# Kernel tuning notes

Measured on AMD Instinct MI355X. Metric: run time of the kernel, lower is better.

Reference implementation:

```python
import jax, jax.numpy as jnp
import numpy as np

B, NIN, NOUT, K = 1024, 126, 126, 3
H1, H2 = 256, 256

def _linear_params(key, out_f, in_f):
    # torch nn.Linear default init: U(-1/sqrt(in_f), 1/sqrt(in_f))
    bound = 1.0 / np.sqrt(in_f)
    kw, kb = jax.random.split(key)
    W = jax.random.uniform(kw, (out_f, in_f), minval=-bound, maxval=bound, dtype=jnp.float32)
    b = jax.random.uniform(kb, (out_f,), minval=-bound, maxval=bound, dtype=jnp.float32)
    return W, b

def setup_inputs() -> dict:
    key = jax.random.key(0)
    k0, k1, k2, kx, ki, ko = jax.random.split(key, 6)
    W0, b0 = _linear_params(k0, H1, NIN)
    W1, b1 = _linear_params(k1, H2, H1)
    W2, b2 = _linear_params(k2, NOUT, H2)
    x = jax.random.normal(kx, (B, NIN), dtype=jnp.float32)
    batch_in_index = jax.random.randint(ki, (B, NIN, K), 0, NIN + 1)   # NIN is zero-pad row
    batch_out_index = jax.random.randint(ko, (B, NOUT, K), 0, NOUT + 1)  # NOUT is zero-pad row
    return dict(x=x, W0=W0, b0=b0, W1=W1, b1=b1, W2=W2, b2=b2,
                batch_in_index=batch_in_index, batch_out_index=batch_out_index)

def reference(x, W0, b0, W1, b1, W2, b2, batch_in_index, batch_out_index):
    # --- layer 0: BatchIndexedLinear with batch_in_index ---
    # padded weight: (nin+1, h1), last row zeros
    pw0 = jnp.concatenate([W0.T, jnp.zeros((1, W0.shape[0]), W0.dtype)], axis=0)
    bw0 = pw0[batch_in_index].sum(-2)                 # (B, nin, h1)
    h = jnp.einsum('bi,bio->bo', x, bw0) + b0          # (B, h1)
    h = jax.nn.elu(h)
    # --- layer 1: plain linear ---
    h = jax.nn.elu(h @ W1.T + b1)                      # (B, h2)
    # --- layer 2: BatchIndexedLinear with batch_out_index ---
    pw2 = jnp.concatenate([W2, jnp.zeros((1, W2.shape[1]), W2.dtype)], axis=0)  # (nout+1, h2)
    g = pw2[batch_out_index].sum(-2)                   # (B, nout, h2)
    pb2 = jnp.concatenate([b2, jnp.zeros((1,), b2.dtype)])
    bb = pb2[batch_out_index].sum(-1)                  # (B, nout)
    return jnp.einsum('bh,boh->bo', h, g) + bb         # (B, nout)
```

## Files before the change

### kernel.cpp

```cpp
#include <hip/hip_runtime.h>

#define B_    1024
#define NIN_  126
#define NOUT_ 126
#define K_    3
#define H1_   256
#define H2_   256
#define RPB   4
#define TPB   512

__device__ __forceinline__ float elu1(float v) { return v > 0.0f ? v : expm1f(v); }

template<int CTRL>
__device__ __forceinline__ float dpp_add(float v) {
    int s = __builtin_amdgcn_update_dpp(0, __float_as_int(v), CTRL, 0xF, 0xF, true);
    return v + __int_as_float(s);
}
__device__ __forceinline__ float qsum8(float v) {
    v = dpp_add<0xB1>(v);
    v = dpp_add<0x4E>(v);
    int s = __builtin_amdgcn_ds_swizzle(__float_as_int(v), 0x101F);
    return v + __int_as_float(s);
}

__device__ __forceinline__ void barrier_lds() {
    asm volatile("s_waitcnt lgkmcnt(0)\n\ts_barrier" ::: "memory");
}

__global__ __launch_bounds__(TPB, 2) void bim_fused(
    const float* __restrict__ x,  const float* __restrict__ W0,
    const float* __restrict__ b0, const float* __restrict__ W1,
    const float* __restrict__ b1, const float* __restrict__ W2,
    const float* __restrict__ b2, const int*  __restrict__ iidx,
    const int*  __restrict__ oidx, float* __restrict__ out)
{
    __shared__ float xe [RPB][128];
    __shared__ float h1s[RPB][H1_];
    __shared__ float h2s[RPB][H2_];
    __shared__ float ts [RPB][128];

    const int tid  = threadIdx.x;
    const int row0 = blockIdx.x * RPB;
    const int q    = tid & 7;
    const int g    = tid >> 3;

    int aj0, aj1, aj2, ar0, ar1, ar2; float ax0, ax1, ax2;
    {
        const int n0 = tid;
        ar0 = n0 / (NIN_ * K_); const int m0 = n0 - ar0 * (NIN_ * K_);
        aj0 = iidx[(row0 + ar0) * (NIN_ * K_) + m0];
        ax0 = x[(row0 + ar0) * NIN_ + m0 / K_];
        const int n1 = tid + TPB;
        ar1 = n1 / (NIN_ * K_); const int m1 = n1 - ar1 * (NIN_ * K_);
        aj1 = iidx[(row0 + ar1) * (NIN_ * K_) + m1];
        ax1 = x[(row0 + ar1) * NIN_ + m1 / K_];
        const int n2 = tid + 2 * TPB;
        const int n2c = n2 < RPB * NIN_ * K_ ? n2 : 0;
        ar2 = n2c / (NIN_ * K_); const int m2 = n2c - ar2 * (NIN_ * K_);
        aj2 = iidx[(row0 + ar2) * (NIN_ * K_) + m2];
        ax2 = x[(row0 + ar2) * NIN_ + m2 / K_];
        if (n2 >= RPB * NIN_ * K_) aj2 = NIN_;
    }
    int ej0, ej1, ej2;
    {
        const int t = tid < RPB * NOUT_ ? tid : 0;
        const int r = t / NOUT_, o = t - r * NOUT_;
        const int base = (row0 + r) * (NOUT_ * K_) + o * K_;
        ej0 = oidx[base]; ej1 = oidx[base + 1]; ej2 = oidx[base + 2];
    }
    float2 wbA[4][4], wbB[4][4];
    #pragma unroll
    for (int oo = 0; oo < 4; ++oo) {
        const float* wp = W0 + (g * 4 + oo) * NIN_;
        #pragma unroll
        for (int jj = 0; jj < 4; ++jj) {
            const int j  = q * 4 + jj * 32;
            const int j2 = (j + 2 > NIN_ - 2) ? (NIN_ - 2) : (j + 2);
            wbA[jj][oo] = *reinterpret_cast<const float2*>(wp + j);
            wbB[jj][oo] = *reinterpret_cast<const float2*>(wp + j2);
        }
    }
    const float4 b0v = *reinterpret_cast<const float4*>(b0 + g * 4);
    const float4 b1v = *reinterpret_cast<const float4*>(b1 + g * 4);
    const int   gD   = (g < 63) ? g : 0;
    const float2 b2v = *reinterpret_cast<const float2*>(b2 + gD * 2);

    (&xe[0][0])[tid] = 0.0f;
    barrier_lds();
    if (aj0 < NIN_) atomicAdd(&xe[ar0][aj0], ax0);
    if (aj1 < NIN_) atomicAdd(&xe[ar1][aj1], ax1);
    if (aj2 < NIN_) atomicAdd(&xe[ar2][aj2], ax2);

    float4 wc[8][4];
    #pragma unroll
    for (int oo = 0; oo < 4; ++oo) {
        const float* wp = W1 + (g * 4 + oo) * H1_;
        #pragma unroll
        for (int jj = 0; jj < 8; ++jj)
            wc[jj][oo] = *reinterpret_cast<const float4*>(wp + q * 4 + jj * 32);
    }
    barrier_lds();

    {
        float acc[4][4] = {};
        #pragma unroll
        for (int jj = 0; jj < 4; ++jj) {
            const int j = q * 4 + jj * 32;
            #pragma unroll
            for (int r = 0; r < RPB; ++r) {
                const float4 a = *reinterpret_cast<const float4*>(&xe[r][j]);
                #pragma unroll
                for (int oo = 0; oo < 4; ++oo) {
                    acc[oo][r] = fmaf(wbA[jj][oo].x, a.x, acc[oo][r]);
                    acc[oo][r] = fmaf(wbA[jj][oo].y, a.y, acc[oo][r]);
                    acc[oo][r] = fmaf(wbB[jj][oo].x, a.z, acc[oo][r]);
                    acc[oo][r] = fmaf(wbB[jj][oo].y, a.w, acc[oo][r]);
                }
            }
        }
        #pragma unroll
        for (int oo = 0; oo < 4; ++oo)
            #pragma unroll
            for (int r = 0; r < RPB; ++r) acc[oo][r] = qsum8(acc[oo][r]);
        float v0 = acc[0][0], v1 = acc[0][1];
        #pragma unroll
        for (int i = 1; i < 8; ++i) {
            v0 = (q == i) ? acc[(2 * i) >> 2][(2 * i) & 3]         : v0;
            v1 = (q == i) ? acc[(2 * i + 1) >> 2][(2 * i + 1) & 3] : v1;
        }
        const int oo = q >> 1, r0 = (q & 1) * 2;
        const float bias = (oo == 0) ? b0v.x : (oo == 1) ? b0v.y : (oo == 2) ? b0v.z : b0v.w;
        const int o = g * 4 + oo;
        h1s[r0][o]     = elu1(v0 + bias);
        h1s[r0 + 1][o] = elu1(v1 + bias);
    }
    barrier_lds();

    float4 wd[8][2];
    {
        float acc[4][4] = {};
        #pragma unroll
        for (int jj = 0; jj < 8; ++jj) {
            const int j = q * 4 + jj * 32;
            #pragma unroll
            for (int r = 0; r < RPB; ++r) {
                const float4 a = *reinterpret_cast<const float4*>(&h1s[r][j]);
                #pragma unroll
                for (int oo = 0; oo < 4; ++oo) {
                    acc[oo][r] = fmaf(wc[jj][oo].x, a.x, acc[oo][r]);
                    acc[oo][r] = fmaf(wc[jj][oo].y, a.y, acc[oo][r]);
                    acc[oo][r] = fmaf(wc[jj][oo].z, a.z, acc[oo][r]);
                    acc[oo][r] = fmaf(wc[jj][oo].w, a.w, acc[oo][r]);
                }
            }
        }
        #pragma unroll
        for (int oo = 0; oo < 2; ++oo) {
            const float* wp = W2 + (gD * 2 + oo) * H2_;
            #pragma unroll
            for (int jj = 0; jj < 8; ++jj)
                wd[jj][oo] = *reinterpret_cast<const float4*>(wp + q * 4 + jj * 32);
        }
        #pragma unroll
        for (int oo = 0; oo < 4; ++oo)
            #pragma unroll
            for (int r = 0; r < RPB; ++r) acc[oo][r] = qsum8(acc[oo][r]);
        float v0 = acc[0][0], v1 = acc[0][1];
        #pragma unroll
        for (int i = 1; i < 8; ++i) {
            v0 = (q == i) ? acc[(2 * i) >> 2][(2 * i) & 3]         : v0;
            v1 = (q == i) ? acc[(2 * i + 1) >> 2][(2 * i + 1) & 3] : v1;
        }
        const int oo = q >> 1, r0 = (q & 1) * 2;
        const float bias = (oo == 0) ? b1v.x : (oo == 1) ? b1v.y : (oo == 2) ? b1v.z : b1v.w;
        const int o = g * 4 + oo;
        h2s[r0][o]     = elu1(v0 + bias);
        h2s[r0 + 1][o] = elu1(v1 + bias);
    }
    barrier_lds();

    {
        float acc[2][4] = {};
        #pragma unroll
        for (int jj = 0; jj < 8; ++jj) {
            const int j = q * 4 + jj * 32;
            #pragma unroll
            for (int r = 0; r < RPB; ++r) {
                const float4 a = *reinterpret_cast<const float4*>(&h2s[r][j]);
                #pragma unroll
                for (int oo = 0; oo < 2; ++oo) {
                    acc[oo][r] = fmaf(wd[jj][oo].x, a.x, acc[oo][r]);
                    acc[oo][r] = fmaf(wd[jj][oo].y, a.y, acc[oo][r]);
                    acc[oo][r] = fmaf(wd[jj][oo].z, a.z, acc[oo][r]);
                    acc[oo][r] = fmaf(wd[jj][oo].w, a.w, acc[oo][r]);
                }
            }
        }
        #pragma unroll
        for (int oo = 0; oo < 2; ++oo)
            #pragma unroll
            for (int r = 0; r < RPB; ++r) acc[oo][r] = qsum8(acc[oo][r]);
        float v = acc[0][0];
        #pragma unroll
        for (int i = 1; i < 8; ++i) v = (q == i) ? acc[i >> 2][i & 3] : v;
        const int oo = q >> 2, rr = q & 3;
        if (g < 63) ts[rr][g * 2 + oo] = v + (oo ? b2v.y : b2v.x);
        else        ts[rr][126 + oo]   = 0.0f;
    }
    barrier_lds();

    if (tid < RPB * NOUT_) {
        const int r = tid / NOUT_, o = tid - r * NOUT_;
        out[(row0 + r) * NOUT_ + o] = ts[r][ej0] + ts[r][ej1] + ts[r][ej2];
    }
}

extern "C" void kernel_launch(void* const* d_in, const int* in_sizes, int n_in,
                              void* d_out, int out_size, void* d_ws, size_t ws_size,
                              hipStream_t stream) {
    const float* x   = (const float*)d_in[0];
    const float* W0  = (const float*)d_in[1];
    const float* b0  = (const float*)d_in[2];
    const float* W1  = (const float*)d_in[3];
    const float* b1  = (const float*)d_in[4];
    const float* W2  = (const float*)d_in[5];
    const float* b2  = (const float*)d_in[6];
    const int*  iidx = (const int*)d_in[7];
    const int*  oidx = (const int*)d_in[8];
    float* out = (float*)d_out;

    bim_fused<<<B_ / RPB, TPB, 0, stream>>>(x, W0, b0, W1, b1, W2, b2, iidx, oidx, out);
}
```

Baseline: 16.33 us.

## Stream weight tiles with one-step register prefetch instead of bulk preloading

The kernel used to load each layer's whole weight slice into registers up front. It now loads one 32-column chunk at a time and prefetches the next chunk while the current one is used in FMAs. It also drops the min-blocks hint from launch_bounds. This cuts register pressure, which could raise occupancy and avoid spills, but it gives up the early overlap of W1 and W2 loads with the previous layer's work and the atomic scatter, so more global load latency may be exposed inside each loop.

```diff
diff --git a/kernel.cpp b/kernel.cpp
--- a/kernel.cpp
+++ b/kernel.cpp
@@ -27,7 +27,7 @@
     asm volatile("s_waitcnt lgkmcnt(0)\n\ts_barrier" ::: "memory");
 }
 
-__global__ __launch_bounds__(TPB, 2) void bim_fused(
+__global__ __launch_bounds__(TPB) void bim_fused(
     const float* __restrict__ x,  const float* __restrict__ W0,
     const float* __restrict__ b0, const float* __restrict__ W1,
     const float* __restrict__ b1, const float* __restrict__ W2,
@@ -68,56 +68,69 @@
         const int base = (row0 + r) * (NOUT_ * K_) + o * K_;
         ej0 = oidx[base]; ej1 = oidx[base + 1]; ej2 = oidx[base + 2];
     }
-    float2 wbA[4][4], wbB[4][4];
-    #pragma unroll
-    for (int oo = 0; oo < 4; ++oo) {
-        const float* wp = W0 + (g * 4 + oo) * NIN_;
-        #pragma unroll
-        for (int jj = 0; jj < 4; ++jj) {
-            const int j  = q * 4 + jj * 32;
-            const int j2 = (j + 2 > NIN_ - 2) ? (NIN_ - 2) : (j + 2);
-            wbA[jj][oo] = *reinterpret_cast<const float2*>(wp + j);
-            wbB[jj][oo] = *reinterpret_cast<const float2*>(wp + j2);
-        }
-    }
     const float4 b0v = *reinterpret_cast<const float4*>(b0 + g * 4);
     const float4 b1v = *reinterpret_cast<const float4*>(b1 + g * 4);
-    const int   gD   = (g < 63) ? g : 0;
+    const int    gD  = (g < 63) ? g : 0;
     const float2 b2v = *reinterpret_cast<const float2*>(b2 + gD * 2);
+
+    const float* wb = W0 + (g * 4) * NIN_;
+    float2 wA[4], wB[4];
+    {
+        const int j = q * 4;
+        const int j2 = (j + 2 > NIN_ - 2) ? (NIN_ - 2) : (j + 2);
+        #pragma unroll
+        for (int oo = 0; oo < 4; ++oo) {
+            wA[oo] = *reinterpret_cast<const float2*>(wb + oo * NIN_ + j);
+            wB[oo] = *reinterpret_cast<const float2*>(wb + oo * NIN_ + j2);
+        }
+    }
 
     (&xe[0][0])[tid] = 0.0f;
     barrier_lds();
     if (aj0 < NIN_) atomicAdd(&xe[ar0][aj0], ax0);
     if (aj1 < NIN_) atomicAdd(&xe[ar1][aj1], ax1);
     if (aj2 < NIN_) atomicAdd(&xe[ar2][aj2], ax2);
-
-    float4 wc[8][4];
-    #pragma unroll
-    for (int oo = 0; oo < 4; ++oo) {
-        const float* wp = W1 + (g * 4 + oo) * H1_;
-        #pragma unroll
-        for (int jj = 0; jj < 8; ++jj)
-            wc[jj][oo] = *reinterpret_cast<const float4*>(wp + q * 4 + jj * 32);
-    }
-    barrier_lds();
-
+    barrier_lds();
+
+    const float* wcp = W1 + (g * 4) * H1_ + q * 4;
+    float4 wc[4];
     {
         float acc[4][4] = {};
         #pragma unroll
         for (int jj = 0; jj < 4; ++jj) {
+            float2 nA[4], nB[4];
+            if (jj < 3) {
+                const int j = q * 4 + (jj + 1) * 32;
+                const int j2 = (j + 2 > NIN_ - 2) ? (NIN_ - 2) : (j + 2);
+                #pragma unroll
+                for (int oo = 0; oo < 4; ++oo) {
+                    nA[oo] = *reinterpret_cast<const float2*>(wb + oo * NIN_ + j);
+                    nB[oo] = *reinterpret_cast<const float2*>(wb + oo * NIN_ + j2);
+                }
+            }
             const int j = q * 4 + jj * 32;
-            #pragma unroll
-            for (int r = 0; r < RPB; ++r) {
-                const float4 a = *reinterpret_cast<const float4*>(&xe[r][j]);
-                #pragma unroll
-                for (int oo = 0; oo < 4; ++oo) {
-                    acc[oo][r] = fmaf(wbA[jj][oo].x, a.x, acc[oo][r]);
-                    acc[oo][r] = fmaf(wbA[jj][oo].y, a.y, acc[oo][r]);
-                    acc[oo][r] = fmaf(wbB[jj][oo].x, a.z, acc[oo][r]);
-                    acc[oo][r] = fmaf(wbB[jj][oo].y, a.w, acc[oo][r]);
-                }
-            }
-        }
+            float4 a[RPB];
+            #pragma unroll
+            for (int r = 0; r < RPB; ++r)
+                a[r] = *reinterpret_cast<const float4*>(&xe[r][j]);
+            #pragma unroll
+            for (int oo = 0; oo < 4; ++oo)
+                #pragma unroll
+                for (int r = 0; r < RPB; ++r) {
+                    acc[oo][r] = fmaf(wA[oo].x, a[r].x, acc[oo][r]);
+                    acc[oo][r] = fmaf(wA[oo].y, a[r].y, acc[oo][r]);
+                    acc[oo][r] = fmaf(wB[oo].x, a[r].z, acc[oo][r]);
+                    acc[oo][r] = fmaf(wB[oo].y, a[r].w, acc[oo][r]);
+                }
+            if (jj < 3) {
+                #pragma unroll
+                for (int oo = 0; oo < 4; ++oo) { wA[oo] = nA[oo]; wB[oo] = nB[oo]; }
+            }
+        }
+        #pragma unroll
+        for (int oo = 0; oo < 4; ++oo)
+            wc[oo] = *reinterpret_cast<const float4*>(wcp + oo * H1_);
+
         #pragma unroll
         for (int oo = 0; oo < 4; ++oo)
             #pragma unroll
@@ -136,31 +149,40 @@
     }
     barrier_lds();
 
-    float4 wd[8][2];
+    const float* wdp = W2 + (gD * 2) * H2_ + q * 4;
+    float4 wd[2];
     {
         float acc[4][4] = {};
         #pragma unroll
         for (int jj = 0; jj < 8; ++jj) {
+            float4 nc[4];
+            if (jj < 7) {
+                #pragma unroll
+                for (int oo = 0; oo < 4; ++oo)
+                    nc[oo] = *reinterpret_cast<const float4*>(wcp + oo * H1_ + (jj + 1) * 32);
+            }
             const int j = q * 4 + jj * 32;
-            #pragma unroll
-            for (int r = 0; r < RPB; ++r) {
-                const float4 a = *reinterpret_cast<const float4*>(&h1s[r][j]);
-                #pragma unroll
-                for (int oo = 0; oo < 4; ++oo) {
-                    acc[oo][r] = fmaf(wc[jj][oo].x, a.x, acc[oo][r]);
-                    acc[oo][r] = fmaf(wc[jj][oo].y, a.y, acc[oo][r]);
-                    acc[oo][r] = fmaf(wc[jj][oo].z, a.z, acc[oo][r]);
-                    acc[oo][r] = fmaf(wc[jj][oo].w, a.w, acc[oo][r]);
-                }
-            }
-        }
-        #pragma unroll
-        for (int oo = 0; oo < 2; ++oo) {
-            const float* wp = W2 + (gD * 2 + oo) * H2_;
-            #pragma unroll
-            for (int jj = 0; jj < 8; ++jj)
-                wd[jj][oo] = *reinterpret_cast<const float4*>(wp + q * 4 + jj * 32);
-        }
+            float4 a[RPB];
+            #pragma unroll
+            for (int r = 0; r < RPB; ++r)
+                a[r] = *reinterpret_cast<const float4*>(&h1s[r][j]);
+            #pragma unroll
+            for (int oo = 0; oo < 4; ++oo)
+                #pragma unroll
+                for (int r = 0; r < RPB; ++r) {
+                    acc[oo][r] = fmaf(wc[oo].x, a[r].x, acc[oo][r]);
+                    acc[oo][r] = fmaf(wc[oo].y, a[r].y, acc[oo][r]);
+                    acc[oo][r] = fmaf(wc[oo].z, a[r].z, acc[oo][r]);
+                    acc[oo][r] = fmaf(wc[oo].w, a[r].w, acc[oo][r]);
+                }
+            if (jj < 7) {
+                #pragma unroll
+                for (int oo = 0; oo < 4; ++oo) wc[oo] = nc[oo];
+            }
+        }
+        wd[0] = *reinterpret_cast<const float4*>(wdp);
+        wd[1] = *reinterpret_cast<const float4*>(wdp + H2_);
+
         #pragma unroll
         for (int oo = 0; oo < 4; ++oo)
             #pragma unroll
@@ -183,18 +205,26 @@
         float acc[2][4] = {};
         #pragma unroll
         for (int jj = 0; jj < 8; ++jj) {
+            float4 nd[2];
+            if (jj < 7) {
+                nd[0] = *reinterpret_cast<const float4*>(wdp + (jj + 1) * 32);
+                nd[1] = *reinterpret_cast<const float4*>(wdp + H2_ + (jj + 1) * 32);
+            }
             const int j = q * 4 + jj * 32;
-            #pragma unroll
-            for (int r = 0; r < RPB; ++r) {
-                const float4 a = *reinterpret_cast<const float4*>(&h2s[r][j]);
-                #pragma unroll
-                for (int oo = 0; oo < 2; ++oo) {
-                    acc[oo][r] = fmaf(wd[jj][oo].x, a.x, acc[oo][r]);
-                    acc[oo][r] = fmaf(wd[jj][oo].y, a.y, acc[oo][r]);
-                    acc[oo][r] = fmaf(wd[jj][oo].z, a.z, acc[oo][r]);
-                    acc[oo][r] = fmaf(wd[jj][oo].w, a.w, acc[oo][r]);
-                }
-            }
+            float4 a[RPB];
+            #pragma unroll
+            for (int r = 0; r < RPB; ++r)
+                a[r] = *reinterpret_cast<const float4*>(&h2s[r][j]);
+            #pragma unroll
+            for (int oo = 0; oo < 2; ++oo)
+                #pragma unroll
+                for (int r = 0; r < RPB; ++r) {
+                    acc[oo][r] = fmaf(wd[oo].x, a[r].x, acc[oo][r]);
+                    acc[oo][r] = fmaf(wd[oo].y, a[r].y, acc[oo][r]);
+                    acc[oo][r] = fmaf(wd[oo].z, a[r].z, acc[oo][r]);
+                    acc[oo][r] = fmaf(wd[oo].w, a[r].w, acc[oo][r]);
+                }
+            if (jj < 7) { wd[0] = nd[0]; wd[1] = nd[1]; }
         }
         #pragma unroll
         for (int oo = 0; oo < 2; ++oo)
```

After: 15.83 us. 1.03x faster.

## Convert weights to bf16 in a prepass, halve rows per block, and software-pipeline weight loads

Applied to the files above, without the earlier changes.

Adds a conversion kernel that writes W0, W1 and W2 as bf16 into the workspace. The fused kernel then reads half as many weight bytes, processes 2 rows per block instead of 4 (doubling the grid), raises occupancy via launch bounds, and streams W1/W2 chunks in an interleaved issue/compute order instead of holding them all in registers. This trades a second kernel launch and reduced weight precision for lower register pressure and less weight traffic per block. bf16 rounding of the weights may loosen accuracy against the fp32 reference.

```diff
diff --git a/kernel.cpp b/kernel.cpp
--- a/kernel.cpp
+++ b/kernel.cpp
@@ -6,8 +6,13 @@
 #define K_    3
 #define H1_   256
 #define H2_   256
-#define RPB   4
+#define RPB   2
 #define TPB   512
+
+#define W0BF_OFF 0
+#define W1BF_OFF 32768
+#define W2BF_OFF 98304
+#define WBF_TOTAL 130560
 
 __device__ __forceinline__ float elu1(float v) { return v > 0.0f ? v : expm1f(v); }
 
@@ -22,17 +27,46 @@
     int s = __builtin_amdgcn_ds_swizzle(__float_as_int(v), 0x101F);
     return v + __int_as_float(s);
 }
-
+__device__ __forceinline__ float sel8(int q, float a0, float a1, float a2, float a3,
+                                      float a4, float a5, float a6, float a7) {
+    float v = a0;
+    v = (q == 1) ? a1 : v;  v = (q == 2) ? a2 : v;  v = (q == 3) ? a3 : v;
+    v = (q == 4) ? a4 : v;  v = (q == 5) ? a5 : v;  v = (q == 6) ? a6 : v;
+    v = (q == 7) ? a7 : v;
+    return v;
+}
 __device__ __forceinline__ void barrier_lds() {
     asm volatile("s_waitcnt lgkmcnt(0)\n\ts_barrier" ::: "memory");
 }
-
-__global__ __launch_bounds__(TPB, 2) void bim_fused(
-    const float* __restrict__ x,  const float* __restrict__ W0,
-    const float* __restrict__ b0, const float* __restrict__ W1,
-    const float* __restrict__ b1, const float* __restrict__ W2,
-    const float* __restrict__ b2, const int*  __restrict__ iidx,
-    const int*  __restrict__ oidx, float* __restrict__ out)
+__device__ __forceinline__ unsigned short f2bf(float f) {
+    unsigned u = __float_as_uint(f);
+    u = (u + 0x7FFFu + ((u >> 16) & 1u)) >> 16;
+    return (unsigned short)u;
+}
+__device__ __forceinline__ float2 bf2f(unsigned u) {
+    return make_float2(__uint_as_float(u << 16), __uint_as_float(u & 0xFFFF0000u));
+}
+
+__global__ __launch_bounds__(256) void wconv(
+    const float* __restrict__ W0, const float* __restrict__ W1,
+    const float* __restrict__ W2, unsigned short* __restrict__ wsb)
+{
+    const int t = blockIdx.x * 256 + threadIdx.x;
+    if (t < 32768) {
+        const int o = t >> 7, j = t & 127;
+        wsb[W0BF_OFF + t] = (j < NIN_) ? f2bf(W0[o * NIN_ + j]) : (unsigned short)0;
+    } else if (t < 98304) {
+        wsb[W1BF_OFF + (t - 32768)] = f2bf(W1[t - 32768]);
+    } else if (t < WBF_TOTAL) {
+        wsb[W2BF_OFF + (t - 98304)] = f2bf(W2[t - 98304]);
+    }
+}
+
+__global__ __launch_bounds__(TPB, 4) void bim_fused(
+    const float* __restrict__ x,  const unsigned short* __restrict__ wsb,
+    const float* __restrict__ b0, const float* __restrict__ b1,
+    const float* __restrict__ b2, const int* __restrict__ iidx,
+    const int* __restrict__ oidx, float* __restrict__ out)
 {
     __shared__ float xe [RPB][128];
     __shared__ float h1s[RPB][H1_];
@@ -44,23 +78,40 @@
     const int q    = tid & 7;
     const int g    = tid >> 3;
 
-    int aj0, aj1, aj2, ar0, ar1, ar2; float ax0, ax1, ax2;
+    int aj0, ar0, aj1, ar1; float ax0, ax1;
     {
         const int n0 = tid;
         ar0 = n0 / (NIN_ * K_); const int m0 = n0 - ar0 * (NIN_ * K_);
         aj0 = iidx[(row0 + ar0) * (NIN_ * K_) + m0];
         ax0 = x[(row0 + ar0) * NIN_ + m0 / K_];
         const int n1 = tid + TPB;
-        ar1 = n1 / (NIN_ * K_); const int m1 = n1 - ar1 * (NIN_ * K_);
+        const bool v1 = n1 < RPB * NIN_ * K_;
+        const int n1c = v1 ? n1 : 0;
+        ar1 = n1c / (NIN_ * K_); const int m1 = n1c - ar1 * (NIN_ * K_);
         aj1 = iidx[(row0 + ar1) * (NIN_ * K_) + m1];
         ax1 = x[(row0 + ar1) * NIN_ + m1 / K_];
-        const int n2 = tid + 2 * TPB;
-        const int n2c = n2 < RPB * NIN_ * K_ ? n2 : 0;
-        ar2 = n2c / (NIN_ * K_); const int m2 = n2c - ar2 * (NIN_ * K_);
-        aj2 = iidx[(row0 + ar2) * (NIN_ * K_) + m2];
-        ax2 = x[(row0 + ar2) * NIN_ + m2 / K_];
-        if (n2 >= RPB * NIN_ * K_) aj2 = NIN_;
-    }
+        if (!v1) aj1 = NIN_;
+    }
+
+    const unsigned short* w0b = wsb + W0BF_OFF + (g * 4) * 128 + q * 4;
+    uint2 wb[4][4];
+    #pragma unroll
+    for (int jj = 0; jj < 4; ++jj)
+        #pragma unroll
+        for (int oo = 0; oo < 4; ++oo)
+            wb[jj][oo] = *reinterpret_cast<const uint2*>(w0b + oo * 128 + jj * 32);
+
+    const unsigned short* wcp = wsb + W1BF_OFF + (g * 4) * H1_ + q * 4;
+    uint2 c0[4], c1[4];
+    #pragma unroll
+    for (int oo = 0; oo < 4; ++oo) c0[oo] = *reinterpret_cast<const uint2*>(wcp + oo * H1_);
+    #pragma unroll
+    for (int oo = 0; oo < 4; ++oo) c1[oo] = *reinterpret_cast<const uint2*>(wcp + oo * H1_ + 32);
+
+    const float4 b0v = *reinterpret_cast<const float4*>(b0 + g * 4);
+    const float4 b1v = *reinterpret_cast<const float4*>(b1 + g * 4);
+    const int    gD  = (g < 63) ? g : 0;
+    const float2 b2v = *reinterpret_cast<const float2*>(b2 + gD * 2);
     int ej0, ej1, ej2;
     {
         const int t = tid < RPB * NOUT_ ? tid : 0;
@@ -68,144 +119,133 @@
         const int base = (row0 + r) * (NOUT_ * K_) + o * K_;
         ej0 = oidx[base]; ej1 = oidx[base + 1]; ej2 = oidx[base + 2];
     }
-    float2 wbA[4][4], wbB[4][4];
-    #pragma unroll
-    for (int oo = 0; oo < 4; ++oo) {
-        const float* wp = W0 + (g * 4 + oo) * NIN_;
-        #pragma unroll
-        for (int jj = 0; jj < 4; ++jj) {
-            const int j  = q * 4 + jj * 32;
-            const int j2 = (j + 2 > NIN_ - 2) ? (NIN_ - 2) : (j + 2);
-            wbA[jj][oo] = *reinterpret_cast<const float2*>(wp + j);
-            wbB[jj][oo] = *reinterpret_cast<const float2*>(wp + j2);
-        }
-    }
-    const float4 b0v = *reinterpret_cast<const float4*>(b0 + g * 4);
-    const float4 b1v = *reinterpret_cast<const float4*>(b1 + g * 4);
-    const int   gD   = (g < 63) ? g : 0;
-    const float2 b2v = *reinterpret_cast<const float2*>(b2 + gD * 2);
-
-    (&xe[0][0])[tid] = 0.0f;
+
+    if (tid < RPB * 128) (&xe[0][0])[tid] = 0.0f;
     barrier_lds();
     if (aj0 < NIN_) atomicAdd(&xe[ar0][aj0], ax0);
     if (aj1 < NIN_) atomicAdd(&xe[ar1][aj1], ax1);
-    if (aj2 < NIN_) atomicAdd(&xe[ar2][aj2], ax2);
-
-    float4 wc[8][4];
-    #pragma unroll
-    for (int oo = 0; oo < 4; ++oo) {
-        const float* wp = W1 + (g * 4 + oo) * H1_;
-        #pragma unroll
-        for (int jj = 0; jj < 8; ++jj)
-            wc[jj][oo] = *reinterpret_cast<const float4*>(wp + q * 4 + jj * 32);
-    }
-    barrier_lds();
-
-    {
-        float acc[4][4] = {};
-        #pragma unroll
-        for (int jj = 0; jj < 4; ++jj) {
-            const int j = q * 4 + jj * 32;
-            #pragma unroll
-            for (int r = 0; r < RPB; ++r) {
-                const float4 a = *reinterpret_cast<const float4*>(&xe[r][j]);
-                #pragma unroll
-                for (int oo = 0; oo < 4; ++oo) {
-                    acc[oo][r] = fmaf(wbA[jj][oo].x, a.x, acc[oo][r]);
-                    acc[oo][r] = fmaf(wbA[jj][oo].y, a.y, acc[oo][r]);
-                    acc[oo][r] = fmaf(wbB[jj][oo].x, a.z, acc[oo][r]);
-                    acc[oo][r] = fmaf(wbB[jj][oo].y, a.w, acc[oo][r]);
-                }
-            }
-        }
+    barrier_lds();
+
+#define BSTEP(JJ) { \
+        const float4 a0 = *reinterpret_cast<const float4*>(&xe[0][q * 4 + (JJ) * 32]); \
+        const float4 a1 = *reinterpret_cast<const float4*>(&xe[1][q * 4 + (JJ) * 32]); \
+        _Pragma("unroll") \
+        for (int oo = 0; oo < 4; ++oo) { \
+            const float2 p0 = bf2f(wb[JJ][oo].x); \
+            const float2 p1 = bf2f(wb[JJ][oo].y); \
+            acc[oo][0] = fmaf(p0.x, a0.x, acc[oo][0]); acc[oo][0] = fmaf(p0.y, a0.y, acc[oo][0]); \
+            acc[oo][0] = fmaf(p1.x, a0.z, acc[oo][0]); acc[oo][0] = fmaf(p1.y, a0.w, acc[oo][0]); \
+            acc[oo][1] = fmaf(p0.x, a1.x, acc[oo][1]); acc[oo][1] = fmaf(p0.y, a1.y, acc[oo][1]); \
+            acc[oo][1] = fmaf(p1.x, a1.z, acc[oo][1]); acc[oo][1] = fmaf(p1.y, a1.w, acc[oo][1]); \
+        } }
+#define CSTEP(W, JJ) { \
+        const float4 a0 = *reinterpret_cast<const float4*>(&h1s[0][q * 4 + (JJ) * 32]); \
+        const float4 a1 = *reinterpret_cast<const float4*>(&h1s[1][q * 4 + (JJ) * 32]); \
+        _Pragma("unroll") \
+        for (int oo = 0; oo < 4; ++oo) { \
+            const float2 p0 = bf2f(W[oo].x); \
+            const float2 p1 = bf2f(W[oo].y); \
+            acc[oo][0] = fmaf(p0.x, a0.x, acc[oo][0]); acc[oo][0] = fmaf(p0.y, a0.y, acc[oo][0]); \
+            acc[oo][0] = fmaf(p1.x, a0.z, acc[oo][0]); acc[oo][0] = fmaf(p1.y, a0.w, acc[oo][0]); \
+            acc[oo][1] = fmaf(p0.x, a1.x, acc[oo][1]); acc[oo][1] = fmaf(p0.y, a1.y, acc[oo][1]); \
+            acc[oo][1] = fmaf(p1.x, a1.z, acc[oo][1]); acc[oo][1] = fmaf(p1.y, a1.w, acc[oo][1]); \
+        } }
+#define DSTEP(W, JJ) { \
+        const float4 a0 = *reinterpret_cast<const float4*>(&h2s[0][q * 4 + (JJ) * 32]); \
+        const float4 a1 = *reinterpret_cast<const float4*>(&h2s[1][q * 4 + (JJ) * 32]); \
+        _Pragma("unroll") \
+        for (int oo = 0; oo < 2; ++oo) { \
+            const float2 p0 = bf2f(W[oo].x); \
+            const float2 p1 = bf2f(W[oo].y); \
+            accd[oo][0] = fmaf(p0.x, a0.x, accd[oo][0]); accd[oo][0] = fmaf(p0.y, a0.y, accd[oo][0]); \
+            accd[oo][0] = fmaf(p1.x, a0.z, accd[oo][0]); accd[oo][0] = fmaf(p1.y, a0.w, accd[oo][0]); \
+            accd[oo][1] = fmaf(p0.x, a1.x, accd[oo][1]); accd[oo][1] = fmaf(p0.y, a1.y, accd[oo][1]); \
+            accd[oo][1] = fmaf(p1.x, a1.z, accd[oo][1]); accd[oo][1] = fmaf(p1.y, a1.w, accd[oo][1]); \
+        } }
+#define ISSUE_C(DST, JJ) { _Pragma("unroll") \
+        for (int oo = 0; oo < 4; ++oo) DST[oo] = *reinterpret_cast<const uint2*>(wcp + oo * H1_ + (JJ) * 32); }
+#define ISSUE_D(DST, JJ) { _Pragma("unroll") \
+        for (int oo = 0; oo < 2; ++oo) DST[oo] = *reinterpret_cast<const uint2*>(wdp + oo * H2_ + (JJ) * 32); }
+
+    uint2 c2[4], c3[4];
+    {
+        float acc[4][2] = {};
+        BSTEP(0)
+        ISSUE_C(c2, 2)
+        BSTEP(1)
+        ISSUE_C(c3, 3)
+        BSTEP(2)
+        BSTEP(3)
         #pragma unroll
         for (int oo = 0; oo < 4; ++oo)
             #pragma unroll
             for (int r = 0; r < RPB; ++r) acc[oo][r] = qsum8(acc[oo][r]);
-        float v0 = acc[0][0], v1 = acc[0][1];
-        #pragma unroll
-        for (int i = 1; i < 8; ++i) {
-            v0 = (q == i) ? acc[(2 * i) >> 2][(2 * i) & 3]         : v0;
-            v1 = (q == i) ? acc[(2 * i + 1) >> 2][(2 * i + 1) & 3] : v1;
-        }
-        const int oo = q >> 1, r0 = (q & 1) * 2;
+        const float v = sel8(q, acc[0][0], acc[0][1], acc[1][0], acc[1][1],
+                                acc[2][0], acc[2][1], acc[3][0], acc[3][1]);
+        const int oo = q >> 1, r = q & 1;
         const float bias = (oo == 0) ? b0v.x : (oo == 1) ? b0v.y : (oo == 2) ? b0v.z : b0v.w;
-        const int o = g * 4 + oo;
-        h1s[r0][o]     = elu1(v0 + bias);
-        h1s[r0 + 1][o] = elu1(v1 + bias);
-    }
-    barrier_lds();
-
-    float4 wd[8][2];
-    {
-        float acc[4][4] = {};
-        #pragma unroll
-        for (int jj = 0; jj < 8; ++jj) {
-            const int j = q * 4 + jj * 32;
-            #pragma unroll
-            for (int r = 0; r < RPB; ++r) {
-                const float4 a = *reinterpret_cast<const float4*>(&h1s[r][j]);
-                #pragma unroll
-                for (int oo = 0; oo < 4; ++oo) {
-                    acc[oo][r] = fmaf(wc[jj][oo].x, a.x, acc[oo][r]);
-                    acc[oo][r] = fmaf(wc[jj][oo].y, a.y, acc[oo][r]);
-                    acc[oo][r] = fmaf(wc[jj][oo].z, a.z, acc[oo][r]);
-                    acc[oo][r] = fmaf(wc[jj][oo].w, a.w, acc[oo][r]);
-                }
-            }
-        }
-        #pragma unroll
-        for (int oo = 0; oo < 2; ++oo) {
-            const float* wp = W2 + (gD * 2 + oo) * H2_;
-            #pragma unroll
-            for (int jj = 0; jj < 8; ++jj)
-                wd[jj][oo] = *reinterpret_cast<const float4*>(wp + q * 4 + jj * 32);
-        }
+        h1s[r][g * 4 + oo] = elu1(v + bias);
+    }
+    barrier_lds();
+
+    const unsigned short* wdp = wsb + W2BF_OFF + (gD * 2) * H2_ + q * 4;
+    uint2 c4[4], c5[4], c6[4], c7[4], d0[2], d1[2];
+    {
+        float acc[4][2] = {};
+        CSTEP(c0, 0)
+        ISSUE_C(c4, 4)
+        CSTEP(c1, 1)
+        ISSUE_C(c5, 5)
+        CSTEP(c2, 2)
+        ISSUE_C(c6, 6)
+        CSTEP(c3, 3)
+        ISSUE_C(c7, 7)
+        CSTEP(c4, 4)
+        ISSUE_D(d0, 0)
+        CSTEP(c5, 5)
+        ISSUE_D(d1, 1)
+        CSTEP(c6, 6)
+        CSTEP(c7, 7)
         #pragma unroll
         for (int oo = 0; oo < 4; ++oo)
             #pragma unroll
             for (int r = 0; r < RPB; ++r) acc[oo][r] = qsum8(acc[oo][r]);
-        float v0 = acc[0][0], v1 = acc[0][1];
-        #pragma unroll
-        for (int i = 1; i < 8; ++i) {
-            v0 = (q == i) ? acc[(2 * i) >> 2][(2 * i) & 3]         : v0;
-            v1 = (q == i) ? acc[(2 * i + 1) >> 2][(2 * i + 1) & 3] : v1;
-        }
-        const int oo = q >> 1, r0 = (q & 1) * 2;
+        const float v = sel8(q, acc[0][0], acc[0][1], acc[1][0], acc[1][1],
+                                acc[2][0], acc[2][1], acc[3][0], acc[3][1]);
+        const int oo = q >> 1, r = q & 1;
         const float bias = (oo == 0) ? b1v.x : (oo == 1) ? b1v.y : (oo == 2) ? b1v.z : b1v.w;
-        const int o = g * 4 + oo;
-        h2s[r0][o]     = elu1(v0 + bias);
-        h2s[r0 + 1][o] = elu1(v1 + bias);
-    }
-    barrier_lds();
-
-    {
-        float acc[2][4] = {};
-        #pragma unroll
-        for (int jj = 0; jj < 8; ++jj) {
-            const int j = q * 4 + jj * 32;
-            #pragma unroll
-            for (int r = 0; r < RPB; ++r) {
-                const float4 a = *reinterpret_cast<const float4*>(&h2s[r][j]);
-                #pragma unroll
-                for (int oo = 0; oo < 2; ++oo) {
-                    acc[oo][r] = fmaf(wd[jj][oo].x, a.x, acc[oo][r]);
-                    acc[oo][r] = fmaf(wd[jj][oo].y, a.y, acc[oo][r]);
-                    acc[oo][r] = fmaf(wd[jj][oo].z, a.z, acc[oo][r]);
-                    acc[oo][r] = fmaf(wd[jj][oo].w, a.w, acc[oo][r]);
-                }
-            }
-        }
+        h2s[r][g * 4 + oo] = elu1(v + bias);
+    }
+    barrier_lds();
+
+    {
+        uint2 d2[2], d3[2], d4[2], d5[2], d6[2], d7[2];
+        float accd[2][2] = {};
+        DSTEP(d0, 0)
+        ISSUE_D(d2, 2)
+        DSTEP(d1, 1)
+        ISSUE_D(d3, 3)
+        DSTEP(d2, 2)
+        ISSUE_D(d4, 4)
+        DSTEP(d3, 3)
+        ISSUE_D(d5, 5)
+        DSTEP(d4, 4)
+        ISSUE_D(d6, 6)
+        DSTEP(d5, 5)
+        ISSUE_D(d7, 7)
+        DSTEP(d6, 6)
+        DSTEP(d7, 7)
         #pragma unroll
         for (int oo = 0; oo < 2; ++oo)
             #pragma unroll
-            for (int r = 0; r < RPB; ++r) acc[oo][r] = qsum8(acc[oo][r]);
-        float v = acc[0][0];
-        #pragma unroll
-        for (int i = 1; i < 8; ++i) v = (q == i) ? acc[i >> 2][i & 3] : v;
-        const int oo = q >> 2, rr = q & 3;
-        if (g < 63) ts[rr][g * 2 + oo] = v + (oo ? b2v.y : b2v.x);
-        else        ts[rr][126 + oo]   = 0.0f;
+            for (int r = 0; r < RPB; ++r) accd[oo][r] = qsum8(accd[oo][r]);
+        const float v = sel8(q, accd[0][0], accd[0][1], accd[1][0], accd[1][1],
+                                accd[0][0], accd[0][1], accd[1][0], accd[1][1]);
+        if (q < 4) {
+            const int oo = q >> 1, rr = q & 1;
+            if (g < 63) ts[rr][g * 2 + oo] = v + (oo ? b2v.y : b2v.x);
+            else        ts[rr][126 + oo]   = 0.0f;
+        }
     }
     barrier_lds();
 
@@ -213,6 +253,11 @@
         const int r = tid / NOUT_, o = tid - r * NOUT_;
         out[(row0 + r) * NOUT_ + o] = ts[r][ej0] + ts[r][ej1] + ts[r][ej2];
     }
+#undef BSTEP
+#undef CSTEP
+#undef DSTEP
+#undef ISSUE_C
+#undef ISSUE_D
 }
 
 extern "C" void kernel_launch(void* const* d_in, const int* in_sizes, int n_in,
@@ -228,6 +273,8 @@
     const int*  iidx = (const int*)d_in[7];
     const int*  oidx = (const int*)d_in[8];
     float* out = (float*)d_out;
-
-    bim_fused<<<B_ / RPB, TPB, 0, stream>>>(x, W0, b0, W1, b1, W2, b2, iidx, oidx, out);
-}
+    unsigned short* wsb = (unsigned short*)d_ws;
+
+    wconv<<<512, 256, 0, stream>>>(W0, W1, W2, wsb);
+    bim_fused<<<B_ / RPB, TPB, 0, stream>>>(x, wsb, b0, b1, b2, iidx, oidx, out);
+}
```

Result: slower. 21.39 us (+31.0%).

## Stage W1 through LDS as bf16 with chunked loads overlapped with layer 0

Applied to the files above, without the earlier changes.

Layer 1 weights are no longer held per thread in registers. They are streamed cooperatively from global memory in four coalesced chunks, converted to bf16 and written to a large dynamic LDS buffer. The chunk loads are interleaved with the atomic scatter and the layer-0 FMA steps to hide their latency. Layer 1 then reads packed bf16 weights from LDS. The goal is to cut register pressure and overlap weight traffic with compute, at the cost of bf16 rounding on W1, extra pack/unpack ALU work, and about 150KB of LDS per block, which limits occupancy to one block per CU.

```diff
diff --git a/kernel.cpp b/kernel.cpp
--- a/kernel.cpp
+++ b/kernel.cpp
@@ -8,8 +8,10 @@
 #define H2_   256
 #define RPB   4
 #define TPB   512
-
-__device__ __forceinline__ float elu1(float v) { return v > 0.0f ? v : expm1f(v); }
+#define W1S   276
+#define SMEM_BYTES (256 * W1S * 2 + (RPB * 128 + RPB * H1_ + RPB * H2_ + RPB * 128) * 4)
+
+__device__ __forceinline__ float elu1(float v) { return v > 0.f ? v : expm1f(v); }
 
 template<int CTRL>
 __device__ __forceinline__ float dpp_add(float v) {
@@ -22,27 +24,40 @@
     int s = __builtin_amdgcn_ds_swizzle(__float_as_int(v), 0x101F);
     return v + __int_as_float(s);
 }
-
 __device__ __forceinline__ void barrier_lds() {
     asm volatile("s_waitcnt lgkmcnt(0)\n\ts_barrier" ::: "memory");
 }
-
-__global__ __launch_bounds__(TPB, 2) void bim_fused(
+__device__ __forceinline__ unsigned f2bf(float f) {
+    unsigned u = __float_as_uint(f);
+    return (u + 0x7FFFu + ((u >> 16) & 1u)) >> 16;
+}
+__device__ __forceinline__ unsigned packbf(float a, float b) {
+    return f2bf(a) | (f2bf(b) << 16);
+}
+__device__ __forceinline__ float2 bf2f(unsigned u) {
+    return make_float2(__uint_as_float(u << 16), __uint_as_float(u & 0xFFFF0000u));
+}
+
+__global__ __launch_bounds__(TPB) void bim_fused(
     const float* __restrict__ x,  const float* __restrict__ W0,
     const float* __restrict__ b0, const float* __restrict__ W1,
     const float* __restrict__ b1, const float* __restrict__ W2,
     const float* __restrict__ b2, const int*  __restrict__ iidx,
     const int*  __restrict__ oidx, float* __restrict__ out)
 {
-    __shared__ float xe [RPB][128];
-    __shared__ float h1s[RPB][H1_];
-    __shared__ float h2s[RPB][H2_];
-    __shared__ float ts [RPB][128];
+    extern __shared__ char smem[];
+    unsigned short* w1l = (unsigned short*)smem;
+    float* xe  = (float*)(smem + 256 * W1S * 2);
+    float* h1s = xe  + RPB * 128;
+    float* h2s = h1s + RPB * H1_;
+    float* tsb = h2s + RPB * H2_;
 
     const int tid  = threadIdx.x;
     const int row0 = blockIdx.x * RPB;
     const int q    = tid & 7;
     const int g    = tid >> 3;
+
+    const float4* w1f4 = reinterpret_cast<const float4*>(W1);
 
     int aj0, aj1, aj2, ar0, ar1, ar2; float ax0, ax1, ax2;
     {
@@ -61,6 +76,32 @@
         ax2 = x[(row0 + ar2) * NIN_ + m2 / K_];
         if (n2 >= RPB * NIN_ * K_) aj2 = NIN_;
     }
+
+    const float* wb = W0 + (g * 4) * NIN_;
+    float2 wA[4][4], wB[4][4];
+    #pragma unroll
+    for (int jj = 0; jj < 4; ++jj) {
+        const int j  = q * 4 + jj * 32;
+        const int j2 = (j + 2 > NIN_ - 2) ? (NIN_ - 2) : (j + 2);
+        #pragma unroll
+        for (int oo = 0; oo < 4; ++oo) {
+            wA[jj][oo] = *reinterpret_cast<const float2*>(wb + oo * NIN_ + j);
+            wB[jj][oo] = *reinterpret_cast<const float2*>(wb + oo * NIN_ + j2);
+        }
+    }
+
+    float4 s0[8], s1[8], s2[8], s3[8];
+#define ISSUE_CHUNK(S, P) { _Pragma("unroll") \
+    for (int u = 0; u < 8; ++u) S[u] = w1f4[((P) * 8 + u) * TPB + tid]; }
+#define WRITE_CHUNK(S, P) { _Pragma("unroll") \
+    for (int u = 0; u < 8; ++u) { \
+        const int i4 = ((P) * 8 + u) * TPB + tid; \
+        const int row = i4 >> 6, c4 = i4 & 63; \
+        uint2 pk; pk.x = packbf(S[u].x, S[u].y); pk.y = packbf(S[u].z, S[u].w); \
+        *reinterpret_cast<uint2*>(&w1l[row * W1S + c4 * 4]) = pk; } }
+
+    ISSUE_CHUNK(s0, 0)
+
     int ej0, ej1, ej2;
     {
         const int t = tid < RPB * NOUT_ ? tid : 0;
@@ -68,56 +109,75 @@
         const int base = (row0 + r) * (NOUT_ * K_) + o * K_;
         ej0 = oidx[base]; ej1 = oidx[base + 1]; ej2 = oidx[base + 2];
     }
-    float2 wbA[4][4], wbB[4][4];
-    #pragma unroll
-    for (int oo = 0; oo < 4; ++oo) {
-        const float* wp = W0 + (g * 4 + oo) * NIN_;
-        #pragma unroll
-        for (int jj = 0; jj < 4; ++jj) {
-            const int j  = q * 4 + jj * 32;
-            const int j2 = (j + 2 > NIN_ - 2) ? (NIN_ - 2) : (j + 2);
-            wbA[jj][oo] = *reinterpret_cast<const float2*>(wp + j);
-            wbB[jj][oo] = *reinterpret_cast<const float2*>(wp + j2);
-        }
-    }
     const float4 b0v = *reinterpret_cast<const float4*>(b0 + g * 4);
     const float4 b1v = *reinterpret_cast<const float4*>(b1 + g * 4);
-    const int   gD   = (g < 63) ? g : 0;
+    const int    gD  = (g < 63) ? g : 0;
     const float2 b2v = *reinterpret_cast<const float2*>(b2 + gD * 2);
 
-    (&xe[0][0])[tid] = 0.0f;
-    barrier_lds();
-    if (aj0 < NIN_) atomicAdd(&xe[ar0][aj0], ax0);
-    if (aj1 < NIN_) atomicAdd(&xe[ar1][aj1], ax1);
-    if (aj2 < NIN_) atomicAdd(&xe[ar2][aj2], ax2);
-
-    float4 wc[8][4];
-    #pragma unroll
-    for (int oo = 0; oo < 4; ++oo) {
-        const float* wp = W1 + (g * 4 + oo) * H1_;
-        #pragma unroll
-        for (int jj = 0; jj < 8; ++jj)
-            wc[jj][oo] = *reinterpret_cast<const float4*>(wp + q * 4 + jj * 32);
-    }
-    barrier_lds();
+    xe[tid] = 0.0f;
+    barrier_lds();
+    if (aj0 < NIN_) atomicAdd(&xe[ar0 * 128 + aj0], ax0);
+    if (aj1 < NIN_) atomicAdd(&xe[ar1 * 128 + aj1], ax1);
+    if (aj2 < NIN_) atomicAdd(&xe[ar2 * 128 + aj2], ax2);
+    WRITE_CHUNK(s0, 0)
+    ISSUE_CHUNK(s1, 1)
+    barrier_lds();
+
+#define BSTEP(JJ) { \
+        const int j = q * 4 + (JJ) * 32; \
+        _Pragma("unroll") \
+        for (int r = 0; r < RPB; ++r) { \
+            const float4 a = *reinterpret_cast<const float4*>(&xe[r * 128 + j]); \
+            _Pragma("unroll") \
+            for (int oo = 0; oo < 4; ++oo) { \
+                acc[oo][r] = fmaf(wA[JJ][oo].x, a.x, acc[oo][r]); \
+                acc[oo][r] = fmaf(wA[JJ][oo].y, a.y, acc[oo][r]); \
+                acc[oo][r] = fmaf(wB[JJ][oo].x, a.z, acc[oo][r]); \
+                acc[oo][r] = fmaf(wB[JJ][oo].y, a.w, acc[oo][r]); \
+            } } }
+#define CSTEP(JJ) { \
+        const int j = q * 4 + (JJ) * 32; \
+        float4 a[RPB]; \
+        _Pragma("unroll") \
+        for (int r = 0; r < RPB; ++r) \
+            a[r] = *reinterpret_cast<const float4*>(&h1s[r * H1_ + j]); \
+        _Pragma("unroll") \
+        for (int oo = 0; oo < 4; ++oo) { \
+            const uint2 wv = *reinterpret_cast<const uint2*>(&w1l[(g * 4 + oo) * W1S + j]); \
+            const float2 p0 = bf2f(wv.x), p1 = bf2f(wv.y); \
+            _Pragma("unroll") \
+            for (int r = 0; r < RPB; ++r) { \
+                acc[oo][r] = fmaf(p0.x, a[r].x, acc[oo][r]); \
+                acc[oo][r] = fmaf(p0.y, a[r].y, acc[oo][r]); \
+                acc[oo][r] = fmaf(p1.x, a[r].z, acc[oo][r]); \
+                acc[oo][r] = fmaf(p1.y, a[r].w, acc[oo][r]); \
+            } } }
+#define DSTEP(JJ) { \
+        const int j = q * 4 + (JJ) * 32; \
+        float4 a[RPB]; \
+        _Pragma("unroll") \
+        for (int r = 0; r < RPB; ++r) \
+            a[r] = *reinterpret_cast<const float4*>(&h2s[r * H2_ + j]); \
+        _Pragma("unroll") \
+        for (int oo = 0; oo < 2; ++oo) { \
+            _Pragma("unroll") \
+            for (int r = 0; r < RPB; ++r) { \
+                accd[oo][r] = fmaf(wd[JJ][oo].x, a[r].x, accd[oo][r]); \
+                accd[oo][r] = fmaf(wd[JJ][oo].y, a[r].y, accd[oo][r]); \
+                accd[oo][r] = fmaf(wd[JJ][oo].z, a[r].z, accd[oo][r]); \
+                accd[oo][r] = fmaf(wd[JJ][oo].w, a[r].w, accd[oo][r]); \
+            } } }
 
     {
         float acc[4][4] = {};
-        #pragma unroll
-        for (int jj = 0; jj < 4; ++jj) {
-            const int j = q * 4 + jj * 32;
-            #pragma unroll
-            for (int r = 0; r < RPB; ++r) {
-                const float4 a = *reinterpret_cast<const float4*>(&xe[r][j]);
-                #pragma unroll
-                for (int oo = 0; oo < 4; ++oo) {
-                    acc[oo][r] = fmaf(wbA[jj][oo].x, a.x, acc[oo][r]);
-                    acc[oo][r] = fmaf(wbA[jj][oo].y, a.y, acc[oo][r]);
-                    acc[oo][r] = fmaf(wbB[jj][oo].x, a.z, acc[oo][r]);
-                    acc[oo][r] = fmaf(wbB[jj][oo].y, a.w, acc[oo][r]);
-                }
-            }
-        }
+        BSTEP(0)
+        BSTEP(1)
+        WRITE_CHUNK(s1, 1)
+        ISSUE_CHUNK(s2, 2)
+        BSTEP(2)
+        BSTEP(3)
+        WRITE_CHUNK(s2, 2)
+        ISSUE_CHUNK(s3, 3)
         #pragma unroll
         for (int oo = 0; oo < 4; ++oo)
             #pragma unroll
@@ -131,36 +191,23 @@
         const int oo = q >> 1, r0 = (q & 1) * 2;
         const float bias = (oo == 0) ? b0v.x : (oo == 1) ? b0v.y : (oo == 2) ? b0v.z : b0v.w;
         const int o = g * 4 + oo;
-        h1s[r0][o]     = elu1(v0 + bias);
-        h1s[r0 + 1][o] = elu1(v1 + bias);
-    }
-    barrier_lds();
-
+        h1s[r0 * H1_ + o]       = elu1(v0 + bias);
+        h1s[(r0 + 1) * H1_ + o] = elu1(v1 + bias);
+        WRITE_CHUNK(s3, 3)
+    }
+    const float* wdp = W2 + (gD * 2) * H2_ + q * 4;
     float4 wd[8][2];
+    #pragma unroll
+    for (int jj = 0; jj < 8; ++jj)
+        #pragma unroll
+        for (int oo = 0; oo < 2; ++oo)
+            wd[jj][oo] = *reinterpret_cast<const float4*>(wdp + oo * H2_ + jj * 32);
+    barrier_lds();
+
     {
         float acc[4][4] = {};
-        #pragma unroll
-        for (int jj = 0; jj < 8; ++jj) {
-            const int j = q * 4 + jj * 32;
-            #pragma unroll
-            for (int r = 0; r < RPB; ++r) {
-                const float4 a = *reinterpret_cast<const float4*>(&h1s[r][j]);
-                #pragma unroll
-                for (int oo = 0; oo < 4; ++oo) {
-                    acc[oo][r] = fmaf(wc[jj][oo].x, a.x, acc[oo][r]);
-                    acc[oo][r] = fmaf(wc[jj][oo].y, a.y, acc[oo][r]);
-                    acc[oo][r] = fmaf(wc[jj][oo].z, a.z, acc[oo][r]);
-                    acc[oo][r] = fmaf(wc[jj][oo].w, a.w, acc[oo][r]);
-                }
-            }
-        }
-        #pragma unroll
-        for (int oo = 0; oo < 2; ++oo) {
-            const float* wp = W2 + (gD * 2 + oo) * H2_;
-            #pragma unroll
-            for (int jj = 0; jj < 8; ++jj)
-                wd[jj][oo] = *reinterpret_cast<const float4*>(wp + q * 4 + jj * 32);
-        }
+        CSTEP(0) CSTEP(1) CSTEP(2) CSTEP(3)
+        CSTEP(4) CSTEP(5) CSTEP(6) CSTEP(7)
         #pragma unroll
         for (int oo = 0; oo < 4; ++oo)
             #pragma unroll
@@ -174,45 +221,37 @@
         const int oo = q >> 1, r0 = (q & 1) * 2;
         const float bias = (oo == 0) ? b1v.x : (oo == 1) ? b1v.y : (oo == 2) ? b1v.z : b1v.w;
         const int o = g * 4 + oo;
-        h2s[r0][o]     = elu1(v0 + bias);
-        h2s[r0 + 1][o] = elu1(v1 + bias);
-    }
-    barrier_lds();
-
-    {
-        float acc[2][4] = {};
-        #pragma unroll
-        for (int jj = 0; jj < 8; ++jj) {
-            const int j = q * 4 + jj * 32;
-            #pragma unroll
-            for (int r = 0; r < RPB; ++r) {
-                const float4 a = *reinterpret_cast<const float4*>(&h2s[r][j]);
-                #pragma unroll
-                for (int oo = 0; oo < 2; ++oo) {
-                    acc[oo][r] = fmaf(wd[jj][oo].x, a.x, acc[oo][r]);
-                    acc[oo][r] = fmaf(wd[jj][oo].y, a.y, acc[oo][r]);
-                    acc[oo][r] = fmaf(wd[jj][oo].z, a.z, acc[oo][r]);
-                    acc[oo][r] = fmaf(wd[jj][oo].w, a.w, acc[oo][r]);
-                }
-            }
-        }
+        h2s[r0 * H2_ + o]       = elu1(v0 + bias);
+        h2s[(r0 + 1) * H2_ + o] = elu1(v1 + bias);
+    }
+    barrier_lds();
+
+    {
+        float accd[2][4] = {};
+        DSTEP(0) DSTEP(1) DSTEP(2) DSTEP(3)
+        DSTEP(4) DSTEP(5) DSTEP(6) DSTEP(7)
         #pragma unroll
         for (int oo = 0; oo < 2; ++oo)
             #pragma unroll
-            for (int r = 0; r < RPB; ++r) acc[oo][r] = qsum8(acc[oo][r]);
-        float v = acc[0][0];
-        #pragma unroll
-        for (int i = 1; i < 8; ++i) v = (q == i) ? acc[i >> 2][i & 3] : v;
+            for (int r = 0; r < RPB; ++r) accd[oo][r] = qsum8(accd[oo][r]);
+        float v = accd[0][0];
+        #pragma unroll
+        for (int i = 1; i < 8; ++i) v = (q == i) ? accd[i >> 2][i & 3] : v;
         const int oo = q >> 2, rr = q & 3;
-        if (g < 63) ts[rr][g * 2 + oo] = v + (oo ? b2v.y : b2v.x);
-        else        ts[rr][126 + oo]   = 0.0f;
+        if (g < 63) tsb[rr * 128 + g * 2 + oo] = v + (oo ? b2v.y : b2v.x);
+        else        tsb[rr * 128 + 126 + oo]   = 0.0f;
     }
     barrier_lds();
 
     if (tid < RPB * NOUT_) {
         const int r = tid / NOUT_, o = tid - r * NOUT_;
-        out[(row0 + r) * NOUT_ + o] = ts[r][ej0] + ts[r][ej1] + ts[r][ej2];
-    }
+        out[(row0 + r) * NOUT_ + o] = tsb[r * 128 + ej0] + tsb[r * 128 + ej1] + tsb[r * 128 + ej2];
+    }
+#undef BSTEP
+#undef CSTEP
+#undef DSTEP
+#undef ISSUE_CHUNK
+#undef WRITE_CHUNK
 }
 
 extern "C" void kernel_launch(void* const* d_in, const int* in_sizes, int n_in,
@@ -229,5 +268,6 @@
     const int*  oidx = (const int*)d_in[8];
     float* out = (float*)d_out;
 
-    bim_fused<<<B_ / RPB, TPB, 0, stream>>>(x, W0, b0, W1, b1, W2, b2, iidx, oidx, out);
-}
+    bim_fused<<<B_ / RPB, TPB, SMEM_BYTES, stream>>>(
+        x, W0, b0, W1, b1, W2, b2, iidx, oidx, out);
+}
```

Result: slower. 18.33 us (+12.2%).
